# Kernel tuning notes

Hardware: AMD Instinct MI355X
Metric: run time of the kernel (lower is better)

Reference implementation:

```python
import jax, jax.numpy as jnp
import numpy as np

Q = 0.8  # quantile used for frequency thresholding


def dct_mat(N, dtype=jnp.float32):
    """Orthonormal DCT-II matrix M, so dct(v) = M @ v and idct(u) = M.T @ u."""
    n = jnp.arange(N)
    k = n[:, None]
    M = jnp.cos(jnp.pi * (2 * n[None, :] + 1) * k / (2 * N))
    s = jnp.full((N,), jnp.sqrt(2.0 / N)).at[0].set(jnp.sqrt(1.0 / N))
    return (s[:, None] * M).astype(dtype)


def setup_inputs() -> dict:
    key = jax.random.key(0)
    B, T, C = 64, 576, 1024  # batch, tokens (24x24 patches), ViT-L width
    x = jax.random.normal(key, (B, T, C), dtype=jnp.float32)
    return {"x": x}


def reference(x):
    # Faithful translation of DCTLAVISBlip.dc_transform(x, use_reconstucted_freq=True).
    # Torch works in (T,B,C)/(C,B,T) layouts; math is DCT/IDCT along the token axis,
    # which we express directly on the [B, T, C] layout (outputs already permuted to
    # batch-first, matching the torch returns).
    B, T, C = x.shape
    M = dct_mat(T, x.dtype)
    # DCT-II (ortho) over tokens: freq axis k.  [B, T, C]
    x_dct = jnp.einsum('btc,kt->bkc', x, M)
    # |mean over batch then over channels| per frequency -> (T,)
    x_dct_mean = jnp.abs(x_dct.mean(axis=0).mean(axis=-1))
    threshold = jnp.abs(jnp.quantile(x_dct_mean, Q))
    # Data-dependent truncation index (host-side, as in the torch .item() call).
    idxs = np.where(np.asarray(x_dct_mean > threshold))[0]
    last_index = int(idxs[-1]) if idxs.size > 0 else -1
    x_dct_trunc = x_dct[:, :last_index, :]  # [B, L, C]; last_index=-1 drops 1 row, as in torch
    L = x_dct_trunc.shape[1]
    # IDCT (DCT-III, ortho) on the truncated length-L sequence.
    Mi = dct_mat(L, x.dtype)
    state = jnp.einsum('blc,lk->bkc', x_dct_trunc, Mi).astype(jnp.float16)  # [B, L, C]
    return state, x_dct_trunc
```

## Files before the change

kernel.cpp:

```cpp
#include <hip/hip_runtime.h>
#include <hip/hip_bf16.h>

typedef _Float16 f16;
typedef _Float16 f16x4 __attribute__((ext_vector_type(4)));
typedef _Float16 f16x8 __attribute__((ext_vector_type(8)));
typedef float f32x4 __attribute__((ext_vector_type(4)));

#define B_    64
#define T_    576
#define C_    1024
#define KDIM  576
#define MPAD  640

__device__ __forceinline__ void gload_lds16(const void* g, void* l) {
  __builtin_amdgcn_global_load_lds(
      (__attribute__((address_space(1))) void*)(void*)g,
      (__attribute__((address_space(3))) void*)l, 16, 0, 0);
}

__global__ void gen_mats(f16* __restrict__ Mh, f16* __restrict__ MiTh, int L) {
  int idx = blockIdx.x * 256 + threadIdx.x;
  if (idx >= MPAD * KDIM) return;
  int k = idx / KDIM;
  int t = idx - k * KDIM;
  const float pif = 3.14159265358979323846f;
  float v = 0.0f;
  if (blockIdx.y == 0) {
    if (k < T_) {
      float a = pif * (float)(2 * t + 1);
      a = a * (float)k;
      a = a / 1152.0f;
      float s = (k == 0) ? sqrtf((float)(1.0 / 576.0)) : sqrtf((float)(2.0 / 576.0));
      v = s * cosf(a);
    }
    Mh[idx] = (f16)v;
  } else {
    int l = t;
    if (k < L && l < L) {
      float a = pif * (float)(2 * k + 1);
      a = a * (float)l;
      a = a / (float)(2 * L);
      float s = (l == 0) ? sqrtf((float)(1.0 / (double)L))
                         : sqrtf((float)(2.0 / (double)L));
      v = s * cosf(a);
    }
    MiTh[idx] = (f16)v;
  }
}

__global__ void transpose_f16(const float* __restrict__ x, f16* __restrict__ XTh) {
  __shared__ float tile[64][65];
  const int b = blockIdx.z;
  const int t0 = blockIdx.y * 64, c0 = blockIdx.x * 64;
  const int i = threadIdx.x;
  const float* xp = x + ((size_t)b * T_ + t0) * C_ + c0;
  const int lrow = i >> 4, lcq = (i & 15) * 4;
#pragma unroll
  for (int p = 0; p < 4; ++p) {
    int r = p * 16 + lrow;
    float4 v = *(const float4*)&xp[(size_t)r * C_ + lcq];
    tile[r][lcq + 0] = v.x; tile[r][lcq + 1] = v.y;
    tile[r][lcq + 2] = v.z; tile[r][lcq + 3] = v.w;
  }
  __syncthreads();
  const int tg = (i & 7) * 8, cl = i >> 3;
#pragma unroll
  for (int h = 0; h < 2; ++h) {
    int c = cl + h * 32;
    f16x8 o;
#pragma unroll
    for (int u = 0; u < 8; ++u) o[u] = (f16)tile[tg + u][c];
    *(f16x8*)&XTh[((size_t)b * C_ + c0 + c) * T_ + t0 + tg] = o;
  }
}

template <int STAGE>
__global__ void gemm_f16(const f16* __restrict__ gA, const f16* __restrict__ gB,
                         float* __restrict__ outp, f16* __restrict__ XdTh,
                         int L, int Kpad, int kloop) {
  __shared__ __align__(16) f16 sA[128 * 32];
  __shared__ __align__(16) f16 sB[128 * 32];

  const int tid = threadIdx.x;
  const int lane = tid & 63, wid = tid >> 6;
  const int b = blockIdx.z, mt = blockIdx.y, nt = blockIdx.x;
  const int m0 = mt * 128, n0 = nt * 128;
  const int wr = wid >> 1, wc = wid & 1;
  const int l15 = lane & 15, lg = lane >> 4;

  const f16* bb = gB + (size_t)b * C_ * KDIM;

  f32x4 acc[4][4];
#pragma unroll
  for (int i = 0; i < 4; ++i)
#pragma unroll
    for (int j = 0; j < 4; ++j) acc[i][j] = (f32x4){0.f, 0.f, 0.f, 0.f};

  for (int kt = 0; kt < kloop; kt += 32) {
    __syncthreads();
#pragma unroll
    for (int it = 0; it < 2; ++it) {
      const int o = it * 4096 + tid * 16;
      const int r = o >> 6, cb = o & 63;
      gload_lds16((const char*)gA + ((size_t)(m0 + r) * KDIM + kt) * 2 + cb,
                  (char*)sA + o);
      gload_lds16((const char*)bb + ((size_t)(n0 + r) * KDIM + kt) * 2 + cb,
                  (char*)sB + o);
    }
    __syncthreads();

    f16x8 af[4], bf[4];
#pragma unroll
    for (int i = 0; i < 4; ++i) {
      af[i] = *(const f16x8*)&sA[(wr * 64 + i * 16 + l15) * 32 + lg * 8];
      bf[i] = *(const f16x8*)&sB[(wc * 64 + i * 16 + l15) * 32 + lg * 8];
    }
#pragma unroll
    for (int i = 0; i < 4; ++i)
#pragma unroll
      for (int j = 0; j < 4; ++j)
        acc[i][j] = __builtin_amdgcn_mfma_f32_16x16x32_f16(af[i], bf[j], acc[i][j], 0, 0, 0);
  }

#pragma unroll
  for (int i = 0; i < 4; ++i) {
    const int k0 = m0 + wr * 64 + i * 16 + lg * 4;
#pragma unroll
    for (int j = 0; j < 4; ++j) {
      const int c = n0 + wc * 64 + j * 16 + l15;
      f32x4 v = acc[i][j];
      if constexpr (STAGE == 1) {
        f16x4 hv;
#pragma unroll
        for (int r = 0; r < 4; ++r) {
          const int k = k0 + r;
          float val = (k < L) ? v[r] : 0.0f;
          if (k < L) outp[((size_t)b * L + k) * C_ + c] = val;
          hv[r] = (f16)val;
        }
        if (k0 < Kpad)
          *(f16x4*)&XdTh[((size_t)b * C_ + c) * KDIM + k0] = hv;
      } else {
#pragma unroll
        for (int r = 0; r < 4; ++r) {
          const int k = k0 + r;
          if (k < L)
            outp[((size_t)b * L + k) * C_ + c] = (float)(f16)v[r];
        }
      }
    }
  }
}

extern "C" void kernel_launch(void* const* d_in, const int* in_sizes, int n_in,
                              void* d_out, int out_size, void* d_ws, size_t ws_size,
                              hipStream_t stream) {
  (void)in_sizes; (void)n_in;
  const float* x = (const float*)d_in[0];

  const int L = out_size / (2 * B_ * C_);
  const int Kpad = ((L + 31) / 32) * 32;
  const int mtiles = (Kpad + 127) / 128;
  float* out_state = (float*)d_out;
  float* out_trunc = out_state + (size_t)B_ * L * C_;

  char* w = (char*)d_ws;
  const size_t SZ_XT = (size_t)B_ * C_ * KDIM * sizeof(f16);
  const size_t SZ_M  = (size_t)MPAD * KDIM * sizeof(f16);
  if (ws_size < 2 * SZ_XT + 2 * SZ_M) return;

  f16* XTh  = (f16*)(w);
  f16* XdTh = (f16*)(w + SZ_XT);
  f16* Mh   = (f16*)(w + 2 * SZ_XT);
  f16* MiTh = (f16*)(w + 2 * SZ_XT + SZ_M);

  gen_mats<<<dim3((MPAD * KDIM + 255) / 256, 2), 256, 0, stream>>>(Mh, MiTh, L);
  transpose_f16<<<dim3(C_ / 64, T_ / 64, B_), 256, 0, stream>>>(x, XTh);
  gemm_f16<1><<<dim3(C_ / 128, mtiles, B_), 256, 0, stream>>>(
      Mh, XTh, out_trunc, XdTh, L, Kpad, KDIM);
  gemm_f16<2><<<dim3(C_ / 128, mtiles, B_), 256, 0, stream>>>(
      MiTh, XdTh, out_state, nullptr, L, Kpad, Kpad);
}
```

Baseline: 546.6 us.

## Fold DCT and truncated IDCT into one precomputed matrix, run both GEMMs in parallel

Precomputes G = Mi^T · M_trunc (a 576x576 product, built with split-precision f16 hi/lo MFMA) so that state = G · x can be computed straight from the transposed input. Both output GEMMs then run as independent halves of a single launch, instead of stage two waiting on a round trip through an intermediate f16 XdT buffer. This removes the serial dependency and the intermediate write/read. The cost is a small extra GEMM, more workspace, and a second GEMM whose K dimension is the full 576 rather than the padded L.

New measurement: 530.7 us. -2.9%, faster.

```diff
diff --git a/kernel.cpp b/kernel.cpp
--- a/kernel.cpp
+++ b/kernel.cpp
@@ -18,37 +18,119 @@
       (__attribute__((address_space(3))) void*)l, 16, 0, 0);
 }
 
-__global__ void gen_mats(f16* __restrict__ Mh, f16* __restrict__ MiTh, int L) {
+__global__ void gen_mats(f16* __restrict__ Mh,
+                         f16* __restrict__ MTh, f16* __restrict__ MTl,
+                         f16* __restrict__ MiTh, f16* __restrict__ MiTl, int L) {
   int idx = blockIdx.x * 256 + threadIdx.x;
   if (idx >= MPAD * KDIM) return;
-  int k = idx / KDIM;
-  int t = idx - k * KDIM;
+  int row = idx / KDIM;
+  int col = idx - row * KDIM;
   const float pif = 3.14159265358979323846f;
   float v = 0.0f;
   if (blockIdx.y == 0) {
-    if (k < T_) {
-      float a = pif * (float)(2 * t + 1);
-      a = a * (float)k;
+    if (row < T_) {
+      float a = pif * (float)(2 * col + 1);
+      a = a * (float)row;
       a = a / 1152.0f;
-      float s = (k == 0) ? sqrtf((float)(1.0 / 576.0)) : sqrtf((float)(2.0 / 576.0));
+      float s = (row == 0) ? sqrtf((float)(1.0 / 576.0)) : sqrtf((float)(2.0 / 576.0));
       v = s * cosf(a);
     }
     Mh[idx] = (f16)v;
+  } else if (blockIdx.y == 1) {
+    if (row < T_) {
+      float a = pif * (float)(2 * row + 1);
+      a = a * (float)col;
+      a = a / 1152.0f;
+      float s = (col == 0) ? sqrtf((float)(1.0 / 576.0)) : sqrtf((float)(2.0 / 576.0));
+      v = s * cosf(a);
+    }
+    f16 h = (f16)v;
+    MTh[idx] = h;
+    MTl[idx] = (f16)(v - (float)h);
   } else {
-    int l = t;
-    if (k < L && l < L) {
-      float a = pif * (float)(2 * k + 1);
-      a = a * (float)l;
+    if (row < L && col < L) {
+      float a = pif * (float)(2 * row + 1);
+      a = a * (float)col;
       a = a / (float)(2 * L);
-      float s = (l == 0) ? sqrtf((float)(1.0 / (double)L))
-                         : sqrtf((float)(2.0 / (double)L));
+      float s = (col == 0) ? sqrtf((float)(1.0 / (double)L))
+                           : sqrtf((float)(2.0 / (double)L));
       v = s * cosf(a);
     }
-    MiTh[idx] = (f16)v;
-  }
-}
-
-__global__ void transpose_f16(const float* __restrict__ x, f16* __restrict__ XTh) {
+    f16 h = (f16)v;
+    MiTh[idx] = h;
+    MiTl[idx] = (f16)(v - (float)h);
+  }
+}
+
+__global__ void gemm_G(const f16* __restrict__ gAh, const f16* __restrict__ gAl,
+                       const f16* __restrict__ gBh, const f16* __restrict__ gBl,
+                       f16* __restrict__ G) {
+  __shared__ __align__(16) f16 sAh[128 * 32];
+  __shared__ __align__(16) f16 sAl[128 * 32];
+  __shared__ __align__(16) f16 sBh[128 * 32];
+  __shared__ __align__(16) f16 sBl[128 * 32];
+  const int tid = threadIdx.x, lane = tid & 63, wid = tid >> 6;
+  const int m0 = blockIdx.y * 128, n0 = blockIdx.x * 128;
+  const int wr = wid >> 1, wc = wid & 1;
+  const int l15 = lane & 15, lg = lane >> 4;
+
+  f32x4 acc[4][4];
+#pragma unroll
+  for (int i = 0; i < 4; ++i)
+#pragma unroll
+    for (int j = 0; j < 4; ++j) acc[i][j] = (f32x4){0.f, 0.f, 0.f, 0.f};
+
+  for (int kt = 0; kt < KDIM; kt += 32) {
+    __syncthreads();
+#pragma unroll
+    for (int it = 0; it < 2; ++it) {
+      const int o = it * 4096 + tid * 16;
+      const int r = o >> 6, cb = o & 63;
+      gload_lds16((const char*)gAh + ((size_t)(m0 + r) * KDIM + kt) * 2 + cb, (char*)sAh + o);
+      gload_lds16((const char*)gAl + ((size_t)(m0 + r) * KDIM + kt) * 2 + cb, (char*)sAl + o);
+      gload_lds16((const char*)gBh + ((size_t)(n0 + r) * KDIM + kt) * 2 + cb, (char*)sBh + o);
+      gload_lds16((const char*)gBl + ((size_t)(n0 + r) * KDIM + kt) * 2 + cb, (char*)sBl + o);
+    }
+    __syncthreads();
+
+    f16x8 ah[4], al[4], bh[4], bl[4];
+#pragma unroll
+    for (int i = 0; i < 4; ++i) {
+      const int ra = (wr * 64 + i * 16 + l15) * 32 + lg * 8;
+      ah[i] = *(const f16x8*)&sAh[ra];
+      al[i] = *(const f16x8*)&sAl[ra];
+      const int rb = (wc * 64 + i * 16 + l15) * 32 + lg * 8;
+      bh[i] = *(const f16x8*)&sBh[rb];
+      bl[i] = *(const f16x8*)&sBl[rb];
+    }
+#pragma unroll
+    for (int i = 0; i < 4; ++i)
+#pragma unroll
+      for (int j = 0; j < 4; ++j) {
+        acc[i][j] = __builtin_amdgcn_mfma_f32_16x16x32_f16(ah[i], bh[j], acc[i][j], 0, 0, 0);
+        acc[i][j] = __builtin_amdgcn_mfma_f32_16x16x32_f16(ah[i], bl[j], acc[i][j], 0, 0, 0);
+        acc[i][j] = __builtin_amdgcn_mfma_f32_16x16x32_f16(al[i], bh[j], acc[i][j], 0, 0, 0);
+      }
+  }
+
+#pragma unroll
+  for (int i = 0; i < 4; ++i) {
+    const int t4 = m0 + wr * 64 + i * 16 + lg * 4;
+#pragma unroll
+    for (int j = 0; j < 4; ++j) {
+      const int k = n0 + wc * 64 + j * 16 + l15;
+      if (t4 < T_) {
+        f32x4 v = acc[i][j];
+        f16x4 hv;
+#pragma unroll
+        for (int r = 0; r < 4; ++r) hv[r] = (f16)v[r];
+        *(f16x4*)&G[(size_t)k * KDIM + t4] = hv;
+      }
+    }
+  }
+}
+
+__global__ void transpose_f16(const float* __restrict__ x, f16* __restrict__ XT) {
   __shared__ float tile[64][65];
   const int b = blockIdx.z;
   const int t0 = blockIdx.y * 64, c0 = blockIdx.x * 64;
@@ -70,25 +152,25 @@
     f16x8 o;
 #pragma unroll
     for (int u = 0; u < 8; ++u) o[u] = (f16)tile[tg + u][c];
-    *(f16x8*)&XTh[((size_t)b * C_ + c0 + c) * T_ + t0 + tg] = o;
-  }
-}
-
-template <int STAGE>
-__global__ void gemm_f16(const f16* __restrict__ gA, const f16* __restrict__ gB,
-                         float* __restrict__ outp, f16* __restrict__ XdTh,
-                         int L, int Kpad, int kloop) {
+    *(f16x8*)&XT[((size_t)b * C_ + c0 + c) * T_ + t0 + tg] = o;
+  }
+}
+
+__global__ void gemm_main(const f16* __restrict__ gM, const f16* __restrict__ gG,
+                          const f16* __restrict__ gXT,
+                          float* __restrict__ out_trunc, float* __restrict__ out_state,
+                          int L) {
   __shared__ __align__(16) f16 sA[128 * 32];
   __shared__ __align__(16) f16 sB[128 * 32];
 
-  const int tid = threadIdx.x;
-  const int lane = tid & 63, wid = tid >> 6;
-  const int b = blockIdx.z, mt = blockIdx.y, nt = blockIdx.x;
-  const int m0 = mt * 128, n0 = nt * 128;
+  const int tid = threadIdx.x, lane = tid & 63, wid = tid >> 6;
+  const int z = blockIdx.z, b = z >> 1, stage = z & 1;
+  const int m0 = blockIdx.y * 128, n0 = blockIdx.x * 128;
   const int wr = wid >> 1, wc = wid & 1;
   const int l15 = lane & 15, lg = lane >> 4;
 
-  const f16* bb = gB + (size_t)b * C_ * KDIM;
+  const f16* gA = stage ? gG : gM;
+  const f16* bb = gXT + (size_t)b * C_ * KDIM;
 
   f32x4 acc[4][4];
 #pragma unroll
@@ -96,7 +178,7 @@
 #pragma unroll
     for (int j = 0; j < 4; ++j) acc[i][j] = (f32x4){0.f, 0.f, 0.f, 0.f};
 
-  for (int kt = 0; kt < kloop; kt += 32) {
+  for (int kt = 0; kt < KDIM; kt += 32) {
     __syncthreads();
 #pragma unroll
     for (int it = 0; it < 2; ++it) {
@@ -122,6 +204,7 @@
         acc[i][j] = __builtin_amdgcn_mfma_f32_16x16x32_f16(af[i], bf[j], acc[i][j], 0, 0, 0);
   }
 
+  float* outp = stage ? out_state : out_trunc;
 #pragma unroll
   for (int i = 0; i < 4; ++i) {
     const int k0 = m0 + wr * 64 + i * 16 + lg * 4;
@@ -129,23 +212,13 @@
     for (int j = 0; j < 4; ++j) {
       const int c = n0 + wc * 64 + j * 16 + l15;
       f32x4 v = acc[i][j];
-      if constexpr (STAGE == 1) {
-        f16x4 hv;
-#pragma unroll
-        for (int r = 0; r < 4; ++r) {
-          const int k = k0 + r;
-          float val = (k < L) ? v[r] : 0.0f;
-          if (k < L) outp[((size_t)b * L + k) * C_ + c] = val;
-          hv[r] = (f16)val;
-        }
-        if (k0 < Kpad)
-          *(f16x4*)&XdTh[((size_t)b * C_ + c) * KDIM + k0] = hv;
-      } else {
-#pragma unroll
-        for (int r = 0; r < 4; ++r) {
-          const int k = k0 + r;
-          if (k < L)
-            outp[((size_t)b * L + k) * C_ + c] = (float)(f16)v[r];
+#pragma unroll
+      for (int r = 0; r < 4; ++r) {
+        const int k = k0 + r;
+        if (k < L) {
+          float val = v[r];
+          if (stage) val = (float)(f16)val;
+          outp[((size_t)b * L + k) * C_ + c] = val;
         }
       }
     }
@@ -159,25 +232,28 @@
   const float* x = (const float*)d_in[0];
 
   const int L = out_size / (2 * B_ * C_);
-  const int Kpad = ((L + 31) / 32) * 32;
-  const int mtiles = (Kpad + 127) / 128;
+  const int mtiles = (L + 127) / 128;
   float* out_state = (float*)d_out;
   float* out_trunc = out_state + (size_t)B_ * L * C_;
 
   char* w = (char*)d_ws;
   const size_t SZ_XT = (size_t)B_ * C_ * KDIM * sizeof(f16);
   const size_t SZ_M  = (size_t)MPAD * KDIM * sizeof(f16);
-  if (ws_size < 2 * SZ_XT + 2 * SZ_M) return;
-
-  f16* XTh  = (f16*)(w);
-  f16* XdTh = (f16*)(w + SZ_XT);
-  f16* Mh   = (f16*)(w + 2 * SZ_XT);
-  f16* MiTh = (f16*)(w + 2 * SZ_XT + SZ_M);
-
-  gen_mats<<<dim3((MPAD * KDIM + 255) / 256, 2), 256, 0, stream>>>(Mh, MiTh, L);
-  transpose_f16<<<dim3(C_ / 64, T_ / 64, B_), 256, 0, stream>>>(x, XTh);
-  gemm_f16<1><<<dim3(C_ / 128, mtiles, B_), 256, 0, stream>>>(
-      Mh, XTh, out_trunc, XdTh, L, Kpad, KDIM);
-  gemm_f16<2><<<dim3(C_ / 128, mtiles, B_), 256, 0, stream>>>(
-      MiTh, XdTh, out_state, nullptr, L, Kpad, Kpad);
-}
+  if (ws_size < SZ_XT + 6 * SZ_M) return;
+
+  f16* XT   = (f16*)(w);
+  f16* Mh   = (f16*)(w + SZ_XT);
+  f16* Gh   = (f16*)(w + SZ_XT + 1 * SZ_M);
+  f16* MTh  = (f16*)(w + SZ_XT + 2 * SZ_M);
+  f16* MTl  = (f16*)(w + SZ_XT + 3 * SZ_M);
+  f16* MiTh = (f16*)(w + SZ_XT + 4 * SZ_M);
+  f16* MiTl = (f16*)(w + SZ_XT + 5 * SZ_M);
+
+  gen_mats<<<dim3((MPAD * KDIM + 255) / 256, 3), 256, 0, stream>>>(
+      Mh, MTh, MTl, MiTh, MiTl, L);
+  gemm_G<<<dim3(MPAD / 128, MPAD / 128), 256, 0, stream>>>(
+      MTh, MTl, MiTh, MiTl, Gh);
+  transpose_f16<<<dim3(C_ / 64, T_ / 64, B_), 256, 0, stream>>>(x, XT);
+  gemm_main<<<dim3(C_ / 128, mtiles, 2 * B_), 256, 0, stream>>>(
+      Mh, Gh, XT, out_trunc, out_state, L);
+}
```
